# Performance work log

Hardware: AMD Instinct MI355X
Metric: run time of the kernel (lower is better)

The kernel has to match this reference:

```python
import jax, jax.numpy as jnp
import numpy as np

B, L, C, H, V = 64, 512, 256, 4, 32000
D = C // H
DIL = (1, 2, 4)
WIN = 3
NC = (50, 20)
NEG = -1e9


def setup_inputs() -> dict:
    key = jax.random.key(0)
    ks = jax.random.split(key, 20)
    g = lambda i, shape: jax.random.normal(ks[i], shape, jnp.float32) * 0.05
    Lay = len(DIL)
    x = jax.random.randint(ks[0], (B, L), 0, V)
    emb = g(1, (V, C)).at[0].set(0.0)  # padding_idx=0 row is zero
    return dict(
        x=x, emb=emb, pos=g(2, (L, C)),
        gp_W=g(3, (Lay, C, C)), gp_as=g(4, (Lay, H, D)), gp_ad=g(5, (Lay, H, D)),
        gf_W=g(6, (Lay, C, C)), gf_as=g(7, (Lay, H, D)), gf_ad=g(8, (Lay, H, D)),
        msg_W=g(9, (Lay, C, 2 * C)), msg_b=jnp.zeros((Lay, C), jnp.float32),
        gru_Wih=g(10, (Lay, 3 * C, C)), gru_bih=jnp.zeros((Lay, 3 * C), jnp.float32),
        gru_Whh=g(11, (Lay, 3 * C, C)), gru_bhh=jnp.zeros((Lay, 3 * C), jnp.float32),
        ln_g=jnp.ones((Lay, C), jnp.float32), ln_b=jnp.zeros((Lay, C), jnp.float32),
        pool_w=g(12, (C,)), pool_b=jnp.zeros((), jnp.float32),
        h0_W=g(13, (NC[0], C)), h0_b=jnp.zeros((NC[0],), jnp.float32),
        h1_W=g(14, (NC[1], C)), h1_b=jnp.zeros((NC[1],), jnp.float32),
    )


def _dense_gat(x, W, a_src, a_dst, adj):
    # x: [B,L,C], W: [C_out,C_in], a_*: [H,D], adj: [B,L,L] bool
    b, l, _ = x.shape
    h = jnp.einsum('blc,oc->blo', x, W).reshape(b, l, H, D).transpose(0, 2, 1, 3)  # [B,H,L,D]
    s = jnp.einsum('bhld,hd->bhl', h, a_src)
    d = jnp.einsum('bhld,hd->bhl', h, a_dst)
    e = s[:, :, :, None] + d[:, :, None, :]            # [B,H,L,L]
    e = jnp.where(e > 0, e, 0.2 * e)                   # LeakyReLU(0.2)
    e = jnp.where(adj[:, None, :, :], e, NEG)
    alpha = jax.nn.softmax(e, axis=-1)                 # dropout is identity in eval
    out = jnp.einsum('bhij,bhjd->bhid', alpha, h)
    return out.transpose(0, 2, 1, 3).reshape(b, l, C)


def _forward(x, emb, pos, gp_W, gp_as, gp_ad, gf_W, gf_as, gf_ad,
             msg_W, msg_b, gru_Wih, gru_bih, gru_Whh, gru_bhh,
             ln_g, ln_b, pool_w, pool_b, h0_W, h0_b, h1_W, h1_b):
    mask = x != 0                                      # [B,L]
    mf = mask.astype(jnp.float32)[..., None]           # [B,L,1]
    h = (emb[x] + pos[None, :, :] * mf) * mf
    logical = jnp.clip(jnp.cumsum(mask.astype(jnp.int32), axis=1) - 1, 0)
    valid = mask[:, None, :] & mask[:, :, None]        # [B,L,L]
    eye = jnp.eye(L, dtype=bool)[None]
    for l in range(len(DIL)):
        dil = DIL[l]
        diff = logical[:, :, None] - logical[:, None, :]
        ad = jnp.abs(diff)
        in_win = (ad <= WIN * dil) & (ad % dil == 0)
        adj_p = (valid & in_win & (diff < 0)) | eye
        adj_f = (valid & in_win & (diff > 0)) | eye
        m_p = _dense_gat(h, gp_W[l], gp_as[l], gp_ad[l], adj_p)
        m_f = _dense_gat(h, gf_W[l], gf_as[l], gf_ad[l], adj_f)
        m = jnp.concatenate([m_p, m_f], axis=-1)
        m = jax.nn.relu(jnp.einsum('blk,ck->blc', m, msg_W[l]) + msg_b[l])
        # GRUCell(input=m, hidden=h), PyTorch gate order: r,z,n
        gi = jnp.einsum('blc,gc->blg', m, gru_Wih[l]) + gru_bih[l]
        gh = jnp.einsum('blc,gc->blg', h, gru_Whh[l]) + gru_bhh[l]
        ir, iz, inn = jnp.split(gi, 3, axis=-1)
        hr, hz, hn = jnp.split(gh, 3, axis=-1)
        r = jax.nn.sigmoid(ir + hr)
        z = jax.nn.sigmoid(iz + hz)
        n = jnp.tanh(inn + r * hn)
        h_new = (1.0 - z) * n + z * h
        mu = jnp.mean(h_new, axis=-1, keepdims=True)
        var = jnp.mean(jnp.square(h_new - mu), axis=-1, keepdims=True)
        h_new = (h_new - mu) * jax.lax.rsqrt(var + 1e-5) * ln_g[l] + ln_b[l]
        h = h_new * mf
    # attention pooling over sequence (masked softmax on linear scores)
    sc = jnp.einsum('blc,c->bl', h, pool_w) + pool_b
    sc = jnp.where(mask, sc, NEG)
    a = jax.nn.softmax(sc, axis=-1)
    pooled = jnp.einsum('bl,blc->bc', a, h)            # dropout identity in eval
    o0 = pooled @ h0_W.T + h0_b
    o1 = pooled @ h1_W.T + h1_b
    return jnp.concatenate([o0, o1], axis=-1)          # [B, 50+20]


def reference(x, emb, pos, gp_W, gp_as, gp_ad, gf_W, gf_as, gf_ad,
              msg_W, msg_b, gru_Wih, gru_bih, gru_Whh, gru_bhh,
              ln_g, ln_b, pool_w, pool_b, h0_W, h0_b, h1_W, h1_b):
    return _forward(x, emb, pos, gp_W, gp_as, gp_ad, gf_W, gf_as, gf_ad,
                    msg_W, msg_b, gru_Wih, gru_bih, gru_Whh, gru_bhh,
                    ln_g, ln_b, pool_w, pool_b, h0_W, h0_b, h1_W, h1_b)
```

## Files before the change

### kernel.cpp

```cpp
#include <hip/hip_runtime.h>
#include <math.h>

#define B_ 64
#define L_ 512
#define C_ 256
#define H_ 4
#define LAY 3
#define NEGV -1e9f

#define GF_BIAS  1
#define GF_RELU  2
#define GF_OBF16 4

typedef __attribute__((ext_vector_type(8))) short short8;
typedef __attribute__((ext_vector_type(4))) short short4v;
typedef __attribute__((ext_vector_type(4))) float floatx4;

static __device__ __forceinline__ float rcp_(float x) { return __builtin_amdgcn_rcpf(x); }
static __device__ __forceinline__ float sig_(float x) { return rcp_(1.f + __expf(-x)); }
static __device__ __forceinline__ float tanh_(float x) {
    float e = __expf(2.f * x);
    return 1.f - 2.f * rcp_(e + 1.f);
}

static __device__ __forceinline__ short f2bf(float f) {
    unsigned x = __float_as_uint(f);
    x += 0x7fffu + ((x >> 16) & 1u);
    return (short)(x >> 16);
}
static __device__ __forceinline__ float bf2f(short s) {
    return __uint_as_float(((unsigned)(unsigned short)s) << 16);
}

static __device__ __forceinline__ int tok_swizzle(int blk) {
    int c8 = blk & 7, i = blk >> 3;
    return (c8 + 8 * (i >> 5)) * 128 + (i & 31) * 4;
}

static __device__ __forceinline__ void gl_lds16(const short* g, short* l) {
    __builtin_amdgcn_global_load_lds(
        (const __attribute__((address_space(1))) unsigned int*)g,
        (__attribute__((address_space(3))) unsigned int*)l, 16, 0, 0);
}

__global__ void scan_kernel(const int* __restrict__ x, int* __restrict__ mask,
                            int* __restrict__ logical, int* __restrict__ pol,
                            int* __restrict__ nvalid) {
    int b = blockIdx.x, t = threadIdx.x;
    __shared__ int s[L_];
    int m = (x[b * L_ + t] != 0) ? 1 : 0;
    s[t] = m;
    __syncthreads();
    for (int off = 1; off < L_; off <<= 1) {
        int v = (t >= off) ? s[t - off] : 0;
        __syncthreads();
        s[t] += v;
        __syncthreads();
    }
    int cum = s[t];
    int lg = cum - 1; if (lg < 0) lg = 0;
    mask[b * L_ + t] = m;
    logical[b * L_ + t] = lg;
    if (m) pol[b * L_ + lg] = t;
    if (t == L_ - 1) nvalid[b] = cum;
}

__global__ void embed_kernel(const int* __restrict__ x, const float* __restrict__ emb,
                             const float* __restrict__ pos, short* __restrict__ hb) {
    int t = threadIdx.x;
    int bl = tok_swizzle(blockIdx.x) + (t >> 6);
    int lane = t & 63;
    int xv = x[bl];
    float mf = (xv != 0) ? 1.f : 0.f;
    int l = bl & (L_ - 1);
    float4 e = *(const float4*)&emb[(size_t)xv * C_ + lane * 4];
    float4 p = *(const float4*)&pos[(size_t)l * C_ + lane * 4];
    short4v hv4;
    hv4.x = f2bf((e.x + p.x * mf) * mf);
    hv4.y = f2bf((e.y + p.y * mf) * mf);
    hv4.z = f2bf((e.z + p.z * mf) * mf);
    hv4.w = f2bf((e.w + p.w * mf) * mf);
    *(short4v*)&hb[(size_t)bl * C_ + lane * 4] = hv4;
}

__global__ void f2bf_kernel(const float* __restrict__ s, short* __restrict__ d, int n) {
    int i = blockIdx.x * 256 + threadIdx.x;
    if (i < n) d[i] = f2bf(s[i]);
}

__global__ void prep_wcomb(const float* __restrict__ gpW, const float* __restrict__ gfW,
                           const float* __restrict__ gpas, const float* __restrict__ gpad,
                           const float* __restrict__ gfas, const float* __restrict__ gfad,
                           short* __restrict__ Wc) {
    int i = blockIdx.x * 256 + threadIdx.x;
    if (i >= 3 * 640 * 256) return;
    int k = i & 255;
    int r = (i >> 8) % 640;
    int l = i / (640 * 256);
    float v = 0.f;
    if (r < 256) {
        v = gpW[((size_t)l * 256 + r) * 256 + k];
    } else if (r < 512) {
        v = gfW[((size_t)l * 256 + (r - 256)) * 256 + k];
    } else {
        int n = r - 512;
        if (n < 16) {
            int type = n >> 3, dir = (n >> 2) & 1, hh = n & 3;
            const float* a = type ? (dir ? gfad : gpad) : (dir ? gfas : gpas);
            const float* W = dir ? gfW : gpW;
            for (int j = 0; j < 64; j++) {
                float av = a[l * 256 + hh * 64 + j];
                float wv = W[((size_t)l * 256 + hh * 64 + j) * 256 + k];
                v = fmaf(av, wv, v);
            }
        }
    }
    Wc[i] = f2bf(v);
}

__global__ void prep_gru_i(const float* __restrict__ Wih, const float* __restrict__ Whh,
                           short* __restrict__ Bc) {
    int i = blockIdx.x * 256 + threadIdx.x;
    if (i >= 3 * 1024 * 512) return;
    int k = i & 511, np = (i >> 9) & 1023, l = i >> 19;
    int ch = np >> 2, g = np & 3;
    float v = 0.f;
    if (g < 2) {
        v = (k < 256) ? Wih[((size_t)l * 768 + g * 256 + ch) * 256 + k]
                      : Whh[((size_t)l * 768 + g * 256 + ch) * 256 + (k - 256)];
    } else if (g == 2) {
        if (k < 256) v = Wih[((size_t)l * 768 + 512 + ch) * 256 + k];
    } else {
        if (k >= 256) v = Whh[((size_t)l * 768 + 512 + ch) * 256 + (k - 256)];
    }
    Bc[i] = f2bf(v);
}

__global__ void prep_bias4(const float* __restrict__ bih, const float* __restrict__ bhh,
                           float* __restrict__ bc) {
    int i = blockIdx.x * 256 + threadIdx.x;
    if (i >= 3 * 1024) return;
    int np = i & 1023, l = i >> 10;
    int ch = np >> 2, g = np & 3;
    float v;
    if (g < 2)       v = bih[l * 768 + g * 256 + ch] + bhh[l * 768 + g * 256 + ch];
    else if (g == 2) v = bih[l * 768 + 512 + ch];
    else             v = bhh[l * 768 + 512 + ch];
    bc[i] = v;
}

__global__ __launch_bounds__(256) void bgemm(const short* __restrict__ A0,
                                             const short* __restrict__ Bw,
                                             void* __restrict__ Cout,
                                             const float* __restrict__ bias,
                                             int K, int lda, int ldc, int nstore,
                                             int cbBits, int flags) {
    __shared__ short As[128 * 32];
    __shared__ short Bs[128 * 32];
    const int id = blockIdx.x;
    const int cb = (id >> 3) & ((1 << cbBits) - 1);
    const int rb = (id & 7) + ((id >> (3 + cbBits)) << 3);
    const int tid = threadIdx.x;
    const int wave = tid >> 6, lane = tid & 63;
    const int wm = wave >> 1, wn = wave & 1;
    const size_t arow0 = (size_t)rb * 128;
    const short* Bb = Bw + (size_t)cb * 128 * K;
    floatx4 acc[4][4];
#pragma unroll
    for (int i = 0; i < 4; i++)
#pragma unroll
        for (int j = 0; j < 4; j++) acc[i][j] = (floatx4)0.f;

    const int srow = lane >> 2;
    const int sq = (lane & 3) * 8;
    const int q = lane >> 4, t16 = lane & 15;

    for (int k0 = 0; k0 < K; k0 += 32) {
        const short* Abase = A0 + arow0 * (size_t)lda + k0;
#pragma unroll
        for (int t = 0; t < 2; ++t) {
            int r = (wave * 2 + t) * 16 + srow;
            gl_lds16(Abase + (size_t)r * lda + sq, &As[r * 32 + sq]);
            gl_lds16(Bb + (size_t)r * K + k0 + sq, &Bs[r * 32 + sq]);
        }
        __syncthreads();
        short8 af[4], bfr[4];
#pragma unroll
        for (int mf = 0; mf < 4; mf++)
            af[mf] = *(const short8*)&As[(wm * 64 + mf * 16 + t16) * 32 + q * 8];
#pragma unroll
        for (int nf = 0; nf < 4; nf++)
            bfr[nf] = *(const short8*)&Bs[(wn * 64 + nf * 16 + t16) * 32 + q * 8];
#pragma unroll
        for (int mf = 0; mf < 4; mf++)
#pragma unroll
            for (int nf = 0; nf < 4; nf++)
                acc[nf][mf] = __builtin_amdgcn_mfma_f32_16x16x32_bf16(
                    bfr[nf], af[mf], acc[nf][mf], 0, 0, 0);
        __syncthreads();
    }

    const int rowbase = rb * 128 + wm * 64;
    const int colbase = cb * 128 + wn * 64;
#pragma unroll
    for (int nf = 0; nf < 4; nf++) {
        int col0 = colbase + nf * 16 + q * 4;
        if (col0 >= nstore) continue;
        float4 bv4 = make_float4(0.f, 0.f, 0.f, 0.f);
        if (flags & GF_BIAS) bv4 = *(const float4*)&bias[col0];
#pragma unroll
        for (int mf = 0; mf < 4; mf++) {
            int row = rowbase + mf * 16 + t16;
            float v0 = acc[nf][mf][0] + bv4.x;
            float v1 = acc[nf][mf][1] + bv4.y;
            float v2 = acc[nf][mf][2] + bv4.z;
            float v3 = acc[nf][mf][3] + bv4.w;
            if (flags & GF_RELU) {
                v0 = fmaxf(v0, 0.f); v1 = fmaxf(v1, 0.f);
                v2 = fmaxf(v2, 0.f); v3 = fmaxf(v3, 0.f);
            }
            size_t base = (size_t)row * ldc + col0;
            if (flags & GF_OBF16) {
                short4v pk;
                pk.x = f2bf(v0); pk.y = f2bf(v1); pk.z = f2bf(v2); pk.w = f2bf(v3);
                *(short4v*)&((short*)Cout)[base] = pk;
            } else {
                float4 pk = make_float4(v0, v1, v2, v3);
                *(float4*)&((float*)Cout)[base] = pk;
            }
        }
    }
}

__global__ __launch_bounds__(256) void projssd_bgemm(const short* __restrict__ A0,
                                                     const short* __restrict__ Bw,
                                                     short* __restrict__ hpb2,
                                                     float* __restrict__ Ssd) {
    __shared__ short As[128 * 32];
    __shared__ short Bs[128 * 32];
    const int id = blockIdx.x;
    const int grp = id >> 3;
    const int cb = grp % 5;
    const int rb = (id & 7) + (grp / 5) * 8;
    const int tid = threadIdx.x;
    const int wave = tid >> 6, lane = tid & 63;
    const int wm = wave >> 1, wn = wave & 1;
    const size_t arow0 = (size_t)rb * 128;
    const short* Bb = Bw + (size_t)cb * 128 * 256;
    floatx4 acc[4][4];
#pragma unroll
    for (int i = 0; i < 4; i++)
#pragma unroll
        for (int j = 0; j < 4; j++) acc[i][j] = (floatx4)0.f;

    const int srow = lane >> 2;
    const int sq = (lane & 3) * 8;
    const int q = lane >> 4, t16 = lane & 15;

    for (int k0 = 0; k0 < 256; k0 += 32) {
        const short* Abase = A0 + arow0 * 256 + k0;
#pragma unroll
        for (int t = 0; t < 2; ++t) {
            int r = (wave * 2 + t) * 16 + srow;
            gl_lds16(Abase + (size_t)r * 256 + sq, &As[r * 32 + sq]);
            gl_lds16(Bb + (size_t)r * 256 + k0 + sq, &Bs[r * 32 + sq]);
        }
        __syncthreads();
        short8 af[4], bfr[4];
#pragma unroll
        for (int mf = 0; mf < 4; mf++)
            af[mf] = *(const short8*)&As[(wm * 64 + mf * 16 + t16) * 32 + q * 8];
#pragma unroll
        for (int nf = 0; nf < 4; nf++)
            bfr[nf] = *(const short8*)&Bs[(wn * 64 + nf * 16 + t16) * 32 + q * 8];
#pragma unroll
        for (int mf = 0; mf < 4; mf++)
#pragma unroll
            for (int nf = 0; nf < 4; nf++)
                acc[nf][mf] = __builtin_amdgcn_mfma_f32_16x16x32_bf16(
                    bfr[nf], af[mf], acc[nf][mf], 0, 0, 0);
        __syncthreads();
    }

    const int rowbase = rb * 128 + wm * 64;
    if (cb < 4) {
        const int colbase = cb * 128 + wn * 64;
#pragma unroll
        for (int nf = 0; nf < 4; nf++) {
            int col0 = colbase + nf * 16 + q * 4;
#pragma unroll
            for (int mf = 0; mf < 4; mf++) {
                int row = rowbase + mf * 16 + t16;
                short4v pk;
                pk.x = f2bf(acc[nf][mf][0]);
                pk.y = f2bf(acc[nf][mf][1]);
                pk.z = f2bf(acc[nf][mf][2]);
                pk.w = f2bf(acc[nf][mf][3]);
                *(short4v*)&hpb2[(size_t)row * 512 + col0] = pk;
            }
        }
    } else {
        if (wn == 0) {
            int col0 = q * 4;
            if (col0 < 16) {
#pragma unroll
                for (int mf = 0; mf < 4; mf++) {
                    int row = rowbase + mf * 16 + t16;
                    float4 pk = make_float4(acc[0][mf][0], acc[0][mf][1],
                                            acc[0][mf][2], acc[0][mf][3]);
                    *(float4*)&Ssd[(size_t)row * 16 + col0] = pk;
                }
            }
        }
    }
}

__global__ __launch_bounds__(512, 2) void gru_bgemm(const short* __restrict__ mmb,
                                                    const short* __restrict__ hb_in,
                                                    const short* __restrict__ Bw,
                                                    short* __restrict__ hn2b,
                                                    const float* __restrict__ bias4) {
    __shared__ short lds[2][32768];
    const int id = blockIdx.x;
    const int swz = (id & 7) * 64 + (id >> 3);
    const int rb = swz & 127;
    const int cb = swz >> 7;
    const int tid = threadIdx.x;
    const int wave = tid >> 6, lane = tid & 63;
    const int wm = wave >> 2, wn = wave & 3;
    const int q = lane >> 4, t16 = lane & 15;
    const size_t arow0 = (size_t)rb * 256;
    const short* Bb = Bw + (size_t)cb * 256 * 512;

    floatx4 acc[4][8];
#pragma unroll
    for (int i = 0; i < 4; i++)
#pragma unroll
        for (int j = 0; j < 8; j++) acc[i][j] = (floatx4)0.f;

    auto stage = [&](int t) {
        const short* Asrc = (t < 4) ? (mmb + t * 64) : (hb_in + (t * 64 - 256));
        short* bufA = lds[t & 1];
        short* bufB = lds[t & 1] + 16384;
#pragma unroll
        for (int i = 0; i < 4; ++i) {
            int unit = i * 512 + tid;
            int row = unit >> 3;
            int csw = (unit & 7) ^ (row & 7);
            gl_lds16(Asrc + (arow0 + (size_t)row) * 256 + csw * 8, bufA + unit * 8);
        }
#pragma unroll
        for (int i = 0; i < 4; ++i) {
            int unit = i * 512 + tid;
            int row = unit >> 3;
            int csw = (unit & 7) ^ (row & 7);
            gl_lds16(Bb + (size_t)row * 512 + t * 64 + csw * 8, bufB + unit * 8);
        }
    };

    auto compute = [&](int t) {
        const short* bufA = lds[t & 1];
        const short* bufB = lds[t & 1] + 16384;
#pragma unroll
        for (int ks = 0; ks < 2; ++ks) {
            short8 af[8], bfr[4];
#pragma unroll
            for (int mf = 0; mf < 8; mf++) {
                int row = wm * 128 + mf * 16 + t16;
                int cg = (ks * 4 + q) ^ (row & 7);
                af[mf] = *(const short8*)&bufA[row * 64 + cg * 8];
            }
#pragma unroll
            for (int nf = 0; nf < 4; nf++) {
                int row = wn * 64 + nf * 16 + t16;
                int cg = (ks * 4 + q) ^ (row & 7);
                bfr[nf] = *(const short8*)&bufB[row * 64 + cg * 8];
            }
            __builtin_amdgcn_s_setprio(1);
#pragma unroll
            for (int mf = 0; mf < 8; mf++)
#pragma unroll
                for (int nf = 0; nf < 4; nf++)
                    acc[nf][mf] = __builtin_amdgcn_mfma_f32_16x16x32_bf16(
                        bfr[nf], af[mf], acc[nf][mf], 0, 0, 0);
            __builtin_amdgcn_s_setprio(0);
        }
    };

    stage(0);
    stage(1);

    for (int t = 0; t < 7; ++t) {
        asm volatile("s_waitcnt vmcnt(8)" ::: "memory");
        __builtin_amdgcn_s_barrier();
        asm volatile("" ::: "memory");
        compute(t);
        asm volatile("" ::: "memory");
        __builtin_amdgcn_s_barrier();
        asm volatile("" ::: "memory");
        if (t < 6) stage(t + 2);
    }
    asm volatile("s_waitcnt vmcnt(0)" ::: "memory");
    __builtin_amdgcn_s_barrier();
    asm volatile("" ::: "memory");
    compute(7);

    short* sO = lds[0];
#pragma unroll
    for (int nf = 0; nf < 4; nf++) {
        int chl = wn * 16 + nf * 4 + q;
        int col0 = cb * 256 + wn * 64 + nf * 16 + q * 4;
        float4 bv4 = *(const float4*)&bias4[col0];
#pragma unroll
        for (int mf = 0; mf < 8; mf++) {
            int rowl = wm * 128 + mf * 16 + t16;
            size_t grow = arow0 + rowl;
            float hp = bf2f(hb_in[grow * 256 + cb * 64 + chl]);
            float r = sig_(acc[nf][mf][0] + bv4.x);
            float z = sig_(acc[nf][mf][1] + bv4.y);
            float nv = tanh_((acc[nf][mf][2] + bv4.z) + r * (acc[nf][mf][3] + bv4.w));
            sO[rowl * 72 + chl] = f2bf((1.f - z) * nv + z * hp);
        }
    }
    __syncthreads();
#pragma unroll
    for (int it = 0; it < 4; ++it) {
        int unit = it * 512 + tid;
        int rowl = unit >> 3, ck = unit & 7;
        *(short8*)&hn2b[(arow0 + rowl) * 256 + cb * 64 + ck * 8] =
            *(const short8*)&sO[rowl * 72 + ck * 8];
    }
}

__global__ __launch_bounds__(256) void ln_kernel(
    const short* __restrict__ hn2b, short* __restrict__ hb,
    const int* __restrict__ mask,
    const float* __restrict__ lng, const float* __restrict__ lnb) {
    int t = threadIdx.x;
    int bl = tok_swizzle(blockIdx.x) + (t >> 6);
    int lane = t & 63;
    short4v v4 = *(const short4v*)&hn2b[(size_t)bl * C_ + lane * 4];
    float v[4] = {bf2f(v4.x), bf2f(v4.y), bf2f(v4.z), bf2f(v4.w)};
    float s = (v[0] + v[1]) + (v[2] + v[3]);
    float ss = (v[0] * v[0] + v[1] * v[1]) + (v[2] * v[2] + v[3] * v[3]);
#pragma unroll
    for (int off = 32; off; off >>= 1) {
        s += __shfl_xor(s, off);
        ss += __shfl_xor(ss, off);
    }
    float mu = s * (1.f / 256.f);
    float var = ss * (1.f / 256.f) - mu * mu;
    float rstd = rsqrtf(fmaxf(var, 0.f) + 1e-5f);
    float4 lg = *(const float4*)&lng[lane * 4];
    float4 lb = *(const float4*)&lnb[lane * 4];
    float mfv = mask[bl] ? 1.f : 0.f;
    short4v yb;
    yb.x = f2bf(((v[0] - mu) * rstd * lg.x + lb.x) * mfv);
    yb.y = f2bf(((v[1] - mu) * rstd * lg.y + lb.y) * mfv);
    yb.z = f2bf(((v[2] - mu) * rstd * lg.z + lb.z) * mfv);
    yb.w = f2bf(((v[3] - mu) * rstd * lg.w + lb.w) * mfv);
    *(short4v*)&hb[(size_t)bl * C_ + lane * 4] = yb;
}

__global__ __launch_bounds__(256) void agg_fused(
    const short* __restrict__ hpb2, const float* __restrict__ S,
    const int* __restrict__ mask, const int* __restrict__ logical,
    const int* __restrict__ pol, const int* __restrict__ nvalid,
    short* __restrict__ m, int dil) {
    int t = threadIdx.x;
    int bl = tok_swizzle(blockIdx.x) + (t >> 6);
    int sub = t & 63;
    int dir = sub >> 5;
    int slot = sub & 31;
    int cb = slot * 8;
    int head = slot >> 3;
    int b = bl >> 9;

    int mi = mask[bl];
    int li = logical[bl];
    int nv = nvalid[b];
    int js[3]; int nn = 0;
    if (mi) {
#pragma unroll
        for (int k = 1; k <= 3; k++) {
            int lj = dir ? (li - k * dil) : (li + k * dil);
            if (lj >= 0 && lj < nv) js[nn++] = pol[b * L_ + lj];
        }
    }
    int sn = dir * 4 + head, dn = 8 + sn;
    float si = S[(size_t)bl * 16 + sn];
    float di = S[(size_t)bl * 16 + dn];
    float e0 = si + di; e0 = e0 > 0.f ? e0 : 0.2f * e0;
    float emax = e0, ev[3];
    for (int k = 0; k < nn; k++) {
        float djv = S[((size_t)(b * L_ + js[k])) * 16 + dn];
        float e = si + djv; e = e > 0.f ? e : 0.2f * e;
        ev[k] = e; emax = fmaxf(emax, e);
    }
    float w0 = __expf(e0 - emax), den = w0;
    float wv[3];
    for (int k = 0; k < nn; k++) { wv[k] = __expf(ev[k] - emax); den += wv[k]; }
    float rden = rcp_(den);

    size_t base = (size_t)bl * 512 + dir * 256 + cb;
    short8 vself = *(const short8*)&hpb2[base];
    float o[8];
#pragma unroll
    for (int j = 0; j < 8; j++) o[j] = w0 * bf2f(vself[j]);
    for (int k = 0; k < nn; k++) {
        short8 vn = *(const short8*)&hpb2[((size_t)(b * L_ + js[k])) * 512 + dir * 256 + cb];
#pragma unroll
        for (int j = 0; j < 8; j++) o[j] = fmaf(wv[k], bf2f(vn[j]), o[j]);
    }
    short8 ov;
#pragma unroll
    for (int j = 0; j < 8; j++) ov[j] = f2bf(o[j] * rden);
    *(short8*)&m[base] = ov;
}

__global__ __launch_bounds__(1024) void pool_head_kernel(
    const short* __restrict__ hb, const int* __restrict__ mask,
    const float* __restrict__ pw, const float* __restrict__ pb,
    const float* __restrict__ h0W, const float* __restrict__ h0b,
    const float* __restrict__ h1W, const float* __restrict__ h1b,
    float* __restrict__ out) {
    int b = blockIdx.x;
    int t = threadIdx.x;
    int lane = t & 63, wave = t >> 6;
    __shared__ float sc[L_];
    __shared__ float red[20];
    __shared__ float part[4][C_];
    __shared__ float pooled[C_];

    float4 wv = *(const float4*)&pw[lane * 4];
    for (int l = wave; l < L_; l += 16) {
        short4v hv = *(const short4v*)&hb[((size_t)b * L_ + l) * C_ + lane * 4];
        float p = bf2f(hv.x) * wv.x + bf2f(hv.y) * wv.y
                + bf2f(hv.z) * wv.z + bf2f(hv.w) * wv.w;
#pragma unroll
        for (int off = 32; off; off >>= 1) p += __shfl_down(p, off);
        if (lane == 0) sc[l] = mask[b * L_ + l] ? (p + pb[0]) : NEGV;
    }
    __syncthreads();

    float v = (t < L_) ? sc[t] : NEGV;
    float mx = v;
#pragma unroll
    for (int off = 32; off; off >>= 1) mx = fmaxf(mx, __shfl_down(mx, off));
    if (lane == 0) red[wave] = mx;
    __syncthreads();
    if (t == 0) {
        float g = red[0];
        for (int i = 1; i < 16; i++) g = fmaxf(g, red[i]);
        red[16] = g;
    }
    __syncthreads();
    float gmax = red[16];
    float e = (t < L_) ? __expf(v - gmax) : 0.f;
    float ssum = e;
#pragma unroll
    for (int off = 32; off; off >>= 1) ssum += __shfl_down(ssum, off);
    if (lane == 0) red[wave] = ssum;
    __syncthreads();
    if (t == 0) {
        float g = 0.f;
        for (int i = 0; i < 16; i++) g += red[i];
        red[17] = 1.f / g;
    }
    __syncthreads();
    if (t < L_) sc[t] = e * red[17];
    __syncthreads();

    int g = t >> 8, c = t & 255;
    const short* hrow = &hb[((size_t)b * L_ + g * 128) * C_ + c];
    const float* scg = &sc[g * 128];
    float a0 = 0.f, a1 = 0.f, a2 = 0.f, a3 = 0.f;
    for (int l = 0; l < 128; l += 4) {
        a0 = fmaf(scg[l + 0], bf2f(hrow[(size_t)(l + 0) * C_]), a0);
        a1 = fmaf(scg[l + 1], bf2f(hrow[(size_t)(l + 1) * C_]), a1);
        a2 = fmaf(scg[l + 2], bf2f(hrow[(size_t)(l + 2) * C_]), a2);
        a3 = fmaf(scg[l + 3], bf2f(hrow[(size_t)(l + 3) * C_]), a3);
    }
    part[g][c] = (a0 + a1) + (a2 + a3);
    __syncthreads();
    if (t < C_) pooled[t] = (part[0][t] + part[1][t]) + (part[2][t] + part[3][t]);
    __syncthreads();

    for (int o = wave; o < 70; o += 16) {
        const float* W = (o < 50) ? (h0W + (size_t)o * C_) : (h1W + (size_t)(o - 50) * C_);
        float bb = (o < 50) ? h0b[o] : h1b[o - 50];
        float4 w4 = *(const float4*)&W[lane * 4];
        float4 p4 = *(const float4*)&pooled[lane * 4];
        float s = p4.x * w4.x + p4.y * w4.y + p4.z * w4.z + p4.w * w4.w;
#pragma unroll
        for (int off = 32; off; off >>= 1) s += __shfl_down(s, off);
        if (lane == 0) out[b * 70 + o] = s + bb;
    }
}

extern "C" void kernel_launch(void* const* d_in, const int* in_sizes, int n_in,
                              void* d_out, int out_size, void* d_ws, size_t ws_size,
                              hipStream_t stream) {
    const int*   x    = (const int*)d_in[0];
    const float* emb  = (const float*)d_in[1];
    const float* pos  = (const float*)d_in[2];
    const float* gpW  = (const float*)d_in[3];
    const float* gpas = (const float*)d_in[4];
    const float* gpad = (const float*)d_in[5];
    const float* gfW  = (const float*)d_in[6];
    const float* gfas = (const float*)d_in[7];
    const float* gfad = (const float*)d_in[8];
    const float* msgW = (const float*)d_in[9];
    const float* msgb = (const float*)d_in[10];
    const float* Wih  = (const float*)d_in[11];
    const float* bih  = (const float*)d_in[12];
    const float* Whh  = (const float*)d_in[13];
    const float* bhh  = (const float*)d_in[14];
    const float* lng  = (const float*)d_in[15];
    const float* lnb  = (const float*)d_in[16];
    const float* pw   = (const float*)d_in[17];
    const float* pb   = (const float*)d_in[18];
    const float* h0W  = (const float*)d_in[19];
    const float* h0b  = (const float*)d_in[20];
    const float* h1W  = (const float*)d_in[21];
    const float* h1b  = (const float*)d_in[22];
    float* out = (float*)d_out;

    const size_t MW = 1024 * 1024;
    float* ws = (float*)d_ws;
    short* hn2b = (short*)ws;
    short* hb   = (short*)(ws + 8 * MW);
    short* mmb  = (short*)(ws + 12 * MW);
    float* Ssd  = ws + 12 * MW;
    short* hpb2 = (short*)(ws + 16 * MW);
    short* mb   = (short*)(ws + 24 * MW);
    short* Wcomb = (short*)(ws + 32 * MW);
    short* msgWb = Wcomb + 3 * 640 * 256;
    short* Bcat  = msgWb + 3 * 256 * 512;
    float* bias4 = (float*)(Bcat + 3 * 1024 * 512);
    int* mask    = (int*)(bias4 + 3 * 1024);
    int* logical = mask + B_ * L_;
    int* pol     = logical + B_ * L_;
    int* nvalid  = pol + B_ * L_;

    prep_wcomb<<<(3 * 640 * 256 + 255) / 256, 256, 0, stream>>>(gpW, gfW, gpas, gpad,
                                                                gfas, gfad, Wcomb);
    f2bf_kernel<<<(3 * 256 * 512 + 255) / 256, 256, 0, stream>>>(msgW, msgWb, 3 * 256 * 512);
    prep_gru_i<<<(3 * 1024 * 512 + 255) / 256, 256, 0, stream>>>(Wih, Whh, Bcat);
    prep_bias4<<<12, 256, 0, stream>>>(bih, bhh, bias4);

    scan_kernel<<<B_, L_, 0, stream>>>(x, mask, logical, pol, nvalid);
    embed_kernel<<<B_ * L_ / 4, 256, 0, stream>>>(x, emb, pos, hb);

    const int DILS[LAY] = {1, 2, 4};

    for (int l = 0; l < LAY; l++) {
        int dil = DILS[l];
        projssd_bgemm<<<256 * 5, 256, 0, stream>>>(hb, Wcomb + (size_t)l * 640 * 256,
                                                   hpb2, Ssd);
        agg_fused<<<8192, 256, 0, stream>>>(hpb2, Ssd, mask, logical, pol, nvalid, mb, dil);
        bgemm<<<256 * 2, 256, 0, stream>>>(mb, msgWb + (size_t)l * 256 * 512,
                                           mmb, msgb + l * C_, 512, 512, 256, 256, 1,
                                           GF_BIAS | GF_RELU | GF_OBF16);
        gru_bgemm<<<512, 512, 0, stream>>>(mmb, hb, Bcat + (size_t)l * 1024 * 512,
                                           hn2b, bias4 + l * 1024);
        ln_kernel<<<8192, 256, 0, stream>>>(hn2b, hb, mask, lng + l * C_, lnb + l * C_);
    }

    pool_head_kernel<<<B_, 1024, 0, stream>>>(hb, mask, pw, pb, h0W, h0b, h1W, h1b, out);
}
```

Baseline: 557.1 us.

## Restructure GRU GEMM main loop into quarter-tile ping-pong with staggered half-stage loads

Splits each K-step of the GRU batched GEMM into four quarter MFMA blocks that reuse A/B fragments. Global-to-LDS loads for the next stage are issued in halves between them, separated by barriers, so load issue and LDS reads interleave more finely with MFMA work. It also changes the block-to-tile mapping for better L2 locality and moves the previous-hidden-state load after the gate math. The cost is many more barriers per iteration and a more fragile vmcnt/lgkmcnt accounting that could stall or race.

```diff
diff --git a/kernel.cpp b/kernel.cpp
--- a/kernel.cpp
+++ b/kernel.cpp
@@ -42,6 +42,8 @@
         (const __attribute__((address_space(1))) unsigned int*)g,
         (__attribute__((address_space(3))) unsigned int*)l, 16, 0, 0);
 }
+
+#define CF() asm volatile("" ::: "memory")
 
 __global__ void scan_kernel(const int* __restrict__ x, int* __restrict__ mask,
                             int* __restrict__ logical, int* __restrict__ pol,
@@ -315,6 +317,53 @@
     }
 }
 
+static __device__ __forceinline__ short8 lds_rd8(const short* p) {
+    return *(const short8*)p;
+}
+
+template <int MH>
+static __device__ __forceinline__ void ld_af(const short* bufA, int wm, int q, int t16,
+                                             short8 af[4][2]) {
+#pragma unroll
+    for (int mfl = 0; mfl < 4; ++mfl) {
+        int row = wm * 128 + (MH * 4 + mfl) * 16 + t16;
+#pragma unroll
+        for (int ks = 0; ks < 2; ++ks) {
+            int cg = (ks * 4 + q) ^ (row & 7);
+            af[mfl][ks] = lds_rd8(&bufA[row * 64 + cg * 8]);
+        }
+    }
+}
+
+template <int NH>
+static __device__ __forceinline__ void ld_bf(const short* bufB, int wn, int q, int t16,
+                                             short8 bf[2][2]) {
+#pragma unroll
+    for (int nfl = 0; nfl < 2; ++nfl) {
+        int row = wn * 64 + (NH * 2 + nfl) * 16 + t16;
+#pragma unroll
+        for (int ks = 0; ks < 2; ++ks) {
+            int cg = (ks * 4 + q) ^ (row & 7);
+            bf[nfl][ks] = lds_rd8(&bufB[row * 64 + cg * 8]);
+        }
+    }
+}
+
+template <int MH, int NH>
+static __device__ __forceinline__ void mfma_q(const short8 af[4][2], const short8 bf[2][2],
+                                              floatx4 acc[4][8]) {
+    __builtin_amdgcn_s_setprio(1);
+#pragma unroll
+    for (int ks = 0; ks < 2; ++ks)
+#pragma unroll
+        for (int mfl = 0; mfl < 4; ++mfl)
+#pragma unroll
+            for (int nfl = 0; nfl < 2; ++nfl)
+                acc[NH * 2 + nfl][MH * 4 + mfl] = __builtin_amdgcn_mfma_f32_16x16x32_bf16(
+                    bf[nfl][ks], af[mfl][ks], acc[NH * 2 + nfl][MH * 4 + mfl], 0, 0, 0);
+    __builtin_amdgcn_s_setprio(0);
+}
+
 __global__ __launch_bounds__(512, 2) void gru_bgemm(const short* __restrict__ mmb,
                                                     const short* __restrict__ hb_in,
                                                     const short* __restrict__ Bw,
@@ -322,9 +371,8 @@
                                                     const float* __restrict__ bias4) {
     __shared__ short lds[2][32768];
     const int id = blockIdx.x;
-    const int swz = (id & 7) * 64 + (id >> 3);
-    const int rb = swz & 127;
-    const int cb = swz >> 7;
+    const int rb = 16 * (id & 7) + (id >> 5);
+    const int cb = (id >> 3) & 3;
     const int tid = threadIdx.x;
     const int wave = tid >> 6, lane = tid & 63;
     const int wm = wave >> 2, wn = wave & 3;
@@ -338,74 +386,73 @@
 #pragma unroll
         for (int j = 0; j < 8; j++) acc[i][j] = (floatx4)0.f;
 
-    auto stage = [&](int t) {
-        const short* Asrc = (t < 4) ? (mmb + t * 64) : (hb_in + (t * 64 - 256));
-        short* bufA = lds[t & 1];
-        short* bufB = lds[t & 1] + 16384;
-#pragma unroll
-        for (int i = 0; i < 4; ++i) {
+    auto stageA = [&](int tt, int Hh) {
+        const short* Asrc = (tt < 4) ? (mmb + tt * 64) : (hb_in + (tt - 4) * 64);
+        short* bufA = lds[tt & 1];
+#pragma unroll
+        for (int i = 0; i < 2; ++i) {
             int unit = i * 512 + tid;
-            int row = unit >> 3;
-            int csw = (unit & 7) ^ (row & 7);
-            gl_lds16(Asrc + (arow0 + (size_t)row) * 256 + csw * 8, bufA + unit * 8);
-        }
-#pragma unroll
-        for (int i = 0; i < 4; ++i) {
+            int row = Hh * 128 + (unit >> 3);
+            int cs = (unit & 7) ^ (row & 7);
+            gl_lds16(Asrc + (arow0 + (size_t)row) * 256 + cs * 8,
+                     bufA + Hh * 8192 + unit * 8);
+        }
+    };
+    auto stageB = [&](int tt, int Hh) {
+        short* bufB = lds[tt & 1] + 16384;
+#pragma unroll
+        for (int i = 0; i < 2; ++i) {
             int unit = i * 512 + tid;
-            int row = unit >> 3;
-            int csw = (unit & 7) ^ (row & 7);
-            gl_lds16(Bb + (size_t)row * 512 + t * 64 + csw * 8, bufB + unit * 8);
+            int row = Hh * 128 + (unit >> 3);
+            int cs = (unit & 7) ^ (row & 7);
+            gl_lds16(Bb + (size_t)row * 512 + tt * 64 + cs * 8,
+                     bufB + Hh * 8192 + unit * 8);
         }
     };
 
-    auto compute = [&](int t) {
+    stageA(0, 0); stageB(0, 0); stageA(0, 1); stageB(0, 1);
+    stageA(1, 0); stageB(1, 0); stageA(1, 1); stageB(1, 1);
+    asm volatile("s_waitcnt vmcnt(8)" ::: "memory");
+    CF(); __builtin_amdgcn_s_barrier(); CF();
+
+    short8 af[4][2], b0[2][2], b1[2][2];
+
+#pragma unroll
+    for (int t = 0; t < 8; ++t) {
         const short* bufA = lds[t & 1];
         const short* bufB = lds[t & 1] + 16384;
-#pragma unroll
-        for (int ks = 0; ks < 2; ++ks) {
-            short8 af[8], bfr[4];
-#pragma unroll
-            for (int mf = 0; mf < 8; mf++) {
-                int row = wm * 128 + mf * 16 + t16;
-                int cg = (ks * 4 + q) ^ (row & 7);
-                af[mf] = *(const short8*)&bufA[row * 64 + cg * 8];
-            }
-#pragma unroll
-            for (int nf = 0; nf < 4; nf++) {
-                int row = wn * 64 + nf * 16 + t16;
-                int cg = (ks * 4 + q) ^ (row & 7);
-                bfr[nf] = *(const short8*)&bufB[row * 64 + cg * 8];
-            }
-            __builtin_amdgcn_s_setprio(1);
-#pragma unroll
-            for (int mf = 0; mf < 8; mf++)
-#pragma unroll
-                for (int nf = 0; nf < 4; nf++)
-                    acc[nf][mf] = __builtin_amdgcn_mfma_f32_16x16x32_bf16(
-                        bfr[nf], af[mf], acc[nf][mf], 0, 0, 0);
-            __builtin_amdgcn_s_setprio(0);
-        }
-    };
-
-    stage(0);
-    stage(1);
-
-    for (int t = 0; t < 7; ++t) {
-        asm volatile("s_waitcnt vmcnt(8)" ::: "memory");
-        __builtin_amdgcn_s_barrier();
-        asm volatile("" ::: "memory");
-        compute(t);
-        asm volatile("" ::: "memory");
-        __builtin_amdgcn_s_barrier();
-        asm volatile("" ::: "memory");
-        if (t < 6) stage(t + 2);
-    }
-    asm volatile("s_waitcnt vmcnt(0)" ::: "memory");
-    __builtin_amdgcn_s_barrier();
-    asm volatile("" ::: "memory");
-    compute(7);
-
-    short* sO = lds[0];
+
+        ld_af<0>(bufA, wm, q, t16, af);
+        ld_bf<0>(bufB, wn, q, t16, b0);
+        if (t > 0 && t < 7) stageB(t + 1, 0);
+        CF(); __builtin_amdgcn_s_barrier();
+        asm volatile("s_waitcnt lgkmcnt(0)" ::: "memory");
+        mfma_q<0, 0>(af, b0, acc);
+        CF(); __builtin_amdgcn_s_barrier(); CF();
+
+        ld_bf<1>(bufB, wn, q, t16, b1);
+        if (t > 0 && t < 7) stageA(t + 1, 1);
+        CF(); __builtin_amdgcn_s_barrier();
+        asm volatile("s_waitcnt lgkmcnt(0)" ::: "memory");
+        mfma_q<0, 1>(af, b1, acc);
+        CF(); __builtin_amdgcn_s_barrier(); CF();
+
+        ld_af<1>(bufA, wm, q, t16, af);
+        if (t > 0 && t < 7) stageB(t + 1, 1);
+        CF(); __builtin_amdgcn_s_barrier();
+        asm volatile("s_waitcnt lgkmcnt(0)" ::: "memory");
+        mfma_q<1, 1>(af, b1, acc);
+        CF(); __builtin_amdgcn_s_barrier(); CF();
+
+        if (t < 6) stageA(t + 2, 0);
+        CF(); __builtin_amdgcn_s_barrier();
+        mfma_q<1, 0>(af, b0, acc);
+        if (t < 6)       asm volatile("s_waitcnt vmcnt(2)" ::: "memory");
+        else if (t == 6) asm volatile("s_waitcnt vmcnt(0)" ::: "memory");
+        CF(); __builtin_amdgcn_s_barrier(); CF();
+    }
+
+    short* sO = (short*)lds;
 #pragma unroll
     for (int nf = 0; nf < 4; nf++) {
         int chl = wn * 16 + nf * 4 + q;
@@ -415,10 +462,10 @@
         for (int mf = 0; mf < 8; mf++) {
             int rowl = wm * 128 + mf * 16 + t16;
             size_t grow = arow0 + rowl;
-            float hp = bf2f(hb_in[grow * 256 + cb * 64 + chl]);
             float r = sig_(acc[nf][mf][0] + bv4.x);
             float z = sig_(acc[nf][mf][1] + bv4.y);
             float nv = tanh_((acc[nf][mf][2] + bv4.z) + r * (acc[nf][mf][3] + bv4.w));
+            float hp = bf2f(hb_in[grow * 256 + cb * 64 + chl]);
             sO[rowl * 72 + chl] = f2bf((1.f - z) * nv + z * hp);
         }
     }
```

Result: faster. 539.6 us (-3.1%).
